# Kernel tuning notes

Measured on AMD Instinct MI355X. Metric: run time of the kernel, lower is better.

The kernel has to match this reference:

```python
import jax, jax.numpy as jnp
import numpy as np

B, N, DIN, DOUT = 1, 8192, 256, 256
EPS = 1e-8

def setup_inputs() -> dict:
    key = jax.random.key(0)
    kA, kX, k1, k2, k3, k4 = jax.random.split(key, 6)
    A = jax.random.uniform(kA, (B, N, N), dtype=jnp.float32)          # dense adjacency [B,N,N]
    X = jax.random.normal(kX, (B, N, DIN), dtype=jnp.float32)          # node features [B,N,Din]
    s1 = 1.0 / np.sqrt(DIN)
    s2 = 1.0 / np.sqrt(DIN + DOUT)
    W_w = jax.random.uniform(k1, (DIN, DOUT), jnp.float32, -s1, s1)
    b_w = jax.random.uniform(k2, (DOUT,), jnp.float32, -s1, s1)
    W_fc = jax.random.uniform(k3, (DIN + DOUT, DOUT), jnp.float32, -s2, s2)
    b_fc = jax.random.uniform(k4, (DOUT,), jnp.float32, -s2, s2)
    return {"A": A, "X": X, "W_w": W_w, "b_w": b_w, "W_fc": W_fc, "b_fc": b_fc}

def reference(A, X, W_w, b_w, W_fc, b_fc):
    # inputs = relu(weight(X))  [B,N,Dout]
    h = jax.nn.relu(jnp.einsum('bnd,de->bne', X, W_w) + b_w)
    # A[...,None] * inputs[:,None] summed over neighbor dim == matmul (avg pooling)
    pooled = jnp.einsum('bij,bjd->bid', A, h)                # [B,N,Dout]
    size = jnp.sum(A, axis=2, keepdims=True) + EPS           # [B,N,1]
    pooled = pooled / size
    cat = jnp.concatenate([X, pooled], axis=-1)              # [B,N,Din+Dout]
    out = jax.nn.relu(jnp.einsum('bnd,de->bne', cat, W_fc) + b_fc) + EPS
    out = out / (jnp.linalg.norm(out) + EPS)                 # global L2 norm over all elements
    return out
```

## Files before the change

kernel.cpp:

```cpp
#include <hip/hip_runtime.h>
#include <hip/hip_bf16.h>
#include <math.h>

typedef __bf16 bf16;
typedef bf16 bf16x8 __attribute__((ext_vector_type(8)));
typedef bf16 bf16x4 __attribute__((ext_vector_type(4)));
typedef float f32x4 __attribute__((ext_vector_type(4)));

#define N_NODES 8192
#define DIN 256
#define DOUT 256
#define KCAT 512
#define EPSF 1e-8f
#define KSPLIT 4
#define KBLK 2048
#define BM 64
#define BK 32
#define NT (KBLK / BK)
#define BBASE 4096
#define BUFSZ 20480

__device__ __forceinline__ f32x4 mfma16(bf16x8 a, bf16x8 b, f32x4 c) {
    return __builtin_amdgcn_mfma_f32_16x16x32_bf16(a, b, c, 0, 0, 0);
}

#define WAITVM(N) asm volatile("s_waitcnt vmcnt(" #N ")" ::: "memory")
#define WAITLGKM  asm volatile("s_waitcnt lgkmcnt(0)" ::: "memory")
#define BAR       __builtin_amdgcn_s_barrier()

__global__ __launch_bounds__(256) void k0_prep(const float* __restrict__ Ww,
                                               const float* __restrict__ Wfc,
                                               bf16* __restrict__ WwT,
                                               bf16* __restrict__ WfcT) {
    int tid = blockIdx.x * 256 + threadIdx.x;
    if (tid < 256 * 256) {
        int n = tid >> 8, k = tid & 255;
        WwT[n * 256 + k] = (bf16)Ww[k * 256 + n];
    }
    if (tid < 256 * 512) {
        int n = tid >> 9, k = tid & 511;
        WfcT[n * 512 + k] = (bf16)Wfc[k * 256 + n];
    }
}

__global__ __launch_bounds__(128) void k1_h(const float* __restrict__ X,
                                            const bf16* __restrict__ WwT,
                                            const float* __restrict__ bw,
                                            bf16* __restrict__ hT) {
    const int lane = threadIdx.x & 63;
    const int wid  = threadIdx.x >> 6;
    const int m0   = blockIdx.x * 16;
    const int lrow = lane & 15;
    const int lk8  = (lane >> 4) * 8;

    f32x4 acc[8];
#pragma unroll
    for (int i = 0; i < 8; ++i) acc[i] = {0.f, 0.f, 0.f, 0.f};

#pragma unroll
    for (int ks = 0; ks < DIN; ks += 32) {
        const float* xp = X + (size_t)(m0 + lrow) * DIN + ks + lk8;
        f32x4 x0 = *reinterpret_cast<const f32x4*>(xp);
        f32x4 x1 = *reinterpret_cast<const f32x4*>(xp + 4);
        bf16x8 a;
#pragma unroll
        for (int j = 0; j < 4; ++j) { a[j] = (bf16)x0[j]; a[4 + j] = (bf16)x1[j]; }
#pragma unroll
        for (int nb = 0; nb < 8; ++nb) {
            int col = wid * 128 + nb * 16 + lrow;
            bf16x8 b = *reinterpret_cast<const bf16x8*>(WwT + (size_t)col * DIN + ks + lk8);
            acc[nb] = mfma16(a, b, acc[nb]);
        }
    }
    const int mrow = m0 + (lane >> 4) * 4;
#pragma unroll
    for (int nb = 0; nb < 8; ++nb) {
        int col = wid * 128 + nb * 16 + lrow;
        float bias = bw[col];
        bf16x4 hv;
#pragma unroll
        for (int j = 0; j < 4; ++j) {
            float v = acc[nb][j] + bias;
            hv[j] = (bf16)(v > 0.f ? v : 0.f);
        }
        *reinterpret_cast<bf16x4*>(hT + (size_t)col * N_NODES + mrow) = hv;
    }
}

__global__ __launch_bounds__(512, 4) void k2_pool(const float* __restrict__ A,
                                                  const bf16* __restrict__ hT,
                                                  float* __restrict__ part,
                                                  float* __restrict__ rsG) {
    __shared__ __align__(16) unsigned char lds[2][BUFSZ];
    __shared__ float rsp[4][BM];
    const int t    = threadIdx.x;
    const int lane = t & 63;
    const int wid  = t >> 6;
    const int wr   = wid >> 2;
    const int wn   = wid & 3;
    const int lrow = lane & 15;
    const int lk4  = lane >> 4;
    const int mblk = blockIdx.x & 127;
    const int ks   = blockIdx.x >> 7;
    const int m0   = mblk * BM;
    const int kbase = ks * KBLK;

    f32x4 acc[2][4];
    f32x4 sums[2];
#pragma unroll
    for (int i = 0; i < 2; ++i) {
        sums[i] = {0.f, 0.f, 0.f, 0.f};
#pragma unroll
        for (int j = 0; j < 4; ++j) acc[i][j] = {0.f, 0.f, 0.f, 0.f};
    }
    bf16x8 bOne;
#pragma unroll
    for (int j = 0; j < 8; ++j) bOne[j] = (bf16)1.0f;

    const int arow = t >> 3;
    const int apos = t & 7;
    const float* aSrc = A + (size_t)(m0 + arow) * N_NODES + kbase + apos * 4;
    const int awb = arow * 64 + ((((apos >> 1) ^ ((arow >> 1) & 3))) << 4) + (apos & 1) * 8;

    const bf16* bsrc[2];
    int bdst[2];
#pragma unroll
    for (int r = 0; r < 2; ++r) {
        int idx = r * 512 + t;
        int col = idx >> 2;
        int gs  = (idx & 3) ^ ((col >> 1) & 3);
        bsrc[r] = hT + (size_t)col * N_NODES + kbase + gs * 8;
        bdst[r] = BBASE + r * 8192 + wid * 1024;
    }

    int aOff[2], bOff[4];
#pragma unroll
    for (int mf = 0; mf < 2; ++mf) {
        int row = wr * 32 + mf * 16 + lrow;
        aOff[mf] = row * 64 + ((lk4 ^ ((row >> 1) & 3)) << 4);
    }
#pragma unroll
    for (int nf = 0; nf < 4; ++nf) {
        int col = wn * 64 + nf * 16 + lrow;
        bOff[nf] = BBASE + col * 64 + ((lk4 ^ ((col >> 1) & 3)) << 4);
    }

    f32x4 ra;

#define ALOAD(tile) do { ra = *reinterpret_cast<const f32x4*>(aSrc + (size_t)(tile) * BK); } while (0)

#define CVTWRITE(bufidx) do {                                                 \
        bf16x4 w_;                                                            \
        _Pragma("unroll")                                                     \
        for (int j = 0; j < 4; ++j) w_[j] = (bf16)ra[j];                      \
        *reinterpret_cast<bf16x4*>(&lds[bufidx][awb]) = w_;                   \
    } while (0)

#define BDMA(tile, bufidx) do {                                               \
        _Pragma("unroll")                                                     \
        for (int r_ = 0; r_ < 2; ++r_) {                                      \
            __builtin_amdgcn_global_load_lds(                                 \
                (const __attribute__((address_space(1))) void*)(bsrc[r_] + (size_t)(tile) * BK), \
                (__attribute__((address_space(3))) void*)&lds[bufidx][bdst[r_]], \
                16, 0, 0);                                                    \
        }                                                                     \
    } while (0)

#define COMPUTE(bufidx, tile) do {                                            \
        bf16x8 af_[2], bf_[4];                                                \
        _Pragma("unroll")                                                     \
        for (int f = 0; f < 2; ++f)                                           \
            af_[f] = *reinterpret_cast<const bf16x8*>(&lds[bufidx][aOff[f]]); \
        _Pragma("unroll")                                                     \
        for (int f = 0; f < 4; ++f)                                           \
            bf_[f] = *reinterpret_cast<const bf16x8*>(&lds[bufidx][bOff[f]]); \
        _Pragma("unroll")                                                     \
        for (int mf = 0; mf < 2; ++mf)                                        \
            _Pragma("unroll")                                                 \
            for (int nf = 0; nf < 4; ++nf)                                    \
                acc[mf][nf] = mfma16(af_[mf], bf_[nf], acc[mf][nf]);          \
        if (wn == ((tile) & 3)) {                                             \
            sums[0] = mfma16(af_[0], bOne, sums[0]);                          \
            sums[1] = mfma16(af_[1], bOne, sums[1]);                          \
        }                                                                     \
    } while (0)

    ALOAD(0); BDMA(0, 0);
    CVTWRITE(0);
    ALOAD(1); BDMA(1, 1);
    WAITVM(3);
    WAITLGKM;
    BAR;

    for (int tt = 0; tt < NT - 2; ++tt) {
        CVTWRITE((tt + 1) & 1);
        COMPUTE(tt & 1, tt);
        ALOAD(tt + 2);
        WAITVM(1);
        WAITLGKM;
        BAR;
        BDMA(tt + 2, tt & 1);
    }
    CVTWRITE((NT - 1) & 1);
    COMPUTE((NT - 2) & 1, NT - 2);
    WAITVM(0);
    WAITLGKM;
    BAR;
    COMPUTE((NT - 1) & 1, NT - 1);

    if (lrow == 0) {
#pragma unroll
        for (int mf = 0; mf < 2; ++mf)
#pragma unroll
            for (int j = 0; j < 4; ++j)
                rsp[wn][wr * 32 + mf * 16 + lk4 * 4 + j] = sums[mf][j];
    }
    __syncthreads();
    if (t < BM)
        rsG[(size_t)ks * N_NODES + m0 + t] = rsp[0][t] + rsp[1][t] + rsp[2][t] + rsp[3][t];

    float* pp = part + ((size_t)ks * N_NODES + m0) * DOUT;
#pragma unroll
    for (int mf = 0; mf < 2; ++mf)
#pragma unroll
        for (int nf = 0; nf < 4; ++nf) {
            int col = wn * 64 + nf * 16 + lrow;
#pragma unroll
            for (int j = 0; j < 4; ++j) {
                int row = wr * 32 + mf * 16 + lk4 * 4 + j;
                pp[(size_t)row * DOUT + col] = acc[mf][nf][j];
            }
        }
#undef ALOAD
#undef CVTWRITE
#undef BDMA
#undef COMPUTE
}

__global__ __launch_bounds__(256) void k2b_combine(const float* __restrict__ part,
                                                   const float* __restrict__ rsG,
                                                   bf16* __restrict__ pooled) {
    int fl  = blockIdx.x * 256 + threadIdx.x;
    int row = fl >> 6;
    int c4  = (fl & 63) * 4;
    f32x4 s = {0.f, 0.f, 0.f, 0.f};
#pragma unroll
    for (int ks = 0; ks < KSPLIT; ++ks) {
        f32x4 v = *reinterpret_cast<const f32x4*>(part + ((size_t)ks * N_NODES + row) * DOUT + c4);
#pragma unroll
        for (int j = 0; j < 4; ++j) s[j] += v[j];
    }
    float rs = EPSF;
#pragma unroll
    for (int ks = 0; ks < KSPLIT; ++ks) rs += rsG[(size_t)ks * N_NODES + row];
    float inv = 1.f / rs;
    bf16x4 o;
#pragma unroll
    for (int j = 0; j < 4; ++j) o[j] = (bf16)(s[j] * inv);
    *reinterpret_cast<bf16x4*>(pooled + (size_t)row * DOUT + c4) = o;
}

__global__ __launch_bounds__(128) void k3_out(const float* __restrict__ X,
                                              const bf16* __restrict__ pooled,
                                              const bf16* __restrict__ WfcT,
                                              const float* __restrict__ bfc,
                                              float* __restrict__ out,
                                              float* __restrict__ partials) {
    const int lane = threadIdx.x & 63;
    const int wid  = threadIdx.x >> 6;
    const int m0   = blockIdx.x * 16;
    const int lrow = lane & 15;
    const int lk8  = (lane >> 4) * 8;

    f32x4 acc[8];
#pragma unroll
    for (int i = 0; i < 8; ++i) acc[i] = {0.f, 0.f, 0.f, 0.f};

#pragma unroll
    for (int ks = 0; ks < 256; ks += 32) {
        const float* xp = X + (size_t)(m0 + lrow) * DIN + ks + lk8;
        f32x4 x0 = *reinterpret_cast<const f32x4*>(xp);
        f32x4 x1 = *reinterpret_cast<const f32x4*>(xp + 4);
        bf16x8 a;
#pragma unroll
        for (int j = 0; j < 4; ++j) { a[j] = (bf16)x0[j]; a[4 + j] = (bf16)x1[j]; }
#pragma unroll
        for (int nb = 0; nb < 8; ++nb) {
            int col = wid * 128 + nb * 16 + lrow;
            bf16x8 b = *reinterpret_cast<const bf16x8*>(WfcT + (size_t)col * KCAT + ks + lk8);
            acc[nb] = mfma16(a, b, acc[nb]);
        }
    }
#pragma unroll
    for (int ks = 256; ks < 512; ks += 32) {
        bf16x8 a = *reinterpret_cast<const bf16x8*>(pooled + (size_t)(m0 + lrow) * DOUT + (ks - 256) + lk8);
#pragma unroll
        for (int nb = 0; nb < 8; ++nb) {
            int col = wid * 128 + nb * 16 + lrow;
            bf16x8 b = *reinterpret_cast<const bf16x8*>(WfcT + (size_t)col * KCAT + ks + lk8);
            acc[nb] = mfma16(a, b, acc[nb]);
        }
    }

    float ss = 0.f;
#pragma unroll
    for (int nb = 0; nb < 8; ++nb) {
        int col = wid * 128 + nb * 16 + lrow;
        float bias = bfc[col];
#pragma unroll
        for (int j = 0; j < 4; ++j) {
            int row = m0 + (lane >> 4) * 4 + j;
            float v = acc[nb][j] + bias;
            v = (v > 0.f ? v : 0.f) + EPSF;
            out[(size_t)row * DOUT + col] = v;
            ss += v * v;
        }
    }
#pragma unroll
    for (int off = 32; off; off >>= 1) ss += __shfl_xor(ss, off);
    __shared__ float sw[2];
    if (lane == 0) sw[wid] = ss;
    __syncthreads();
    if (threadIdx.x == 0) partials[blockIdx.x] = sw[0] + sw[1];
}

__global__ __launch_bounds__(256) void k4_norm(float* __restrict__ out,
                                               const float* __restrict__ partials) {
    __shared__ float sw[4];
    float s = partials[threadIdx.x] + partials[threadIdx.x + 256];
#pragma unroll
    for (int off = 32; off; off >>= 1) s += __shfl_xor(s, off);
    if ((threadIdx.x & 63) == 0) sw[threadIdx.x >> 6] = s;
    __syncthreads();
    float total = sw[0] + sw[1] + sw[2] + sw[3];
    float scale = 1.f / (sqrtf(total) + EPSF);
    f32x4* o4 = reinterpret_cast<f32x4*>(out);
    const int nvec = N_NODES * DOUT / 4;
    for (int i = blockIdx.x * blockDim.x + threadIdx.x; i < nvec; i += gridDim.x * blockDim.x) {
        f32x4 v = o4[i];
#pragma unroll
        for (int j = 0; j < 4; ++j) v[j] *= scale;
        o4[i] = v;
    }
}

extern "C" void kernel_launch(void* const* d_in, const int* in_sizes, int n_in,
                              void* d_out, int out_size, void* d_ws, size_t ws_size,
                              hipStream_t stream) {
    const float* A   = (const float*)d_in[0];
    const float* X   = (const float*)d_in[1];
    const float* Ww  = (const float*)d_in[2];
    const float* bw  = (const float*)d_in[3];
    const float* Wfc = (const float*)d_in[4];
    const float* bfc = (const float*)d_in[5];
    float* out = (float*)d_out;

    char* ws = (char*)d_ws;
    bf16*  hT        = (bf16*)(ws);
    bf16*  pooled    = (bf16*)(ws + (4u << 20));
    bf16*  WwT       = (bf16*)(ws + (8u << 20));
    bf16*  WfcT      = (bf16*)(ws + (8u << 20) + (128u << 10));
    float* partials  = (float*)(ws + (8u << 20) + (384u << 10));
    float* rsG       = (float*)(ws + (8u << 20) + (512u << 10));
    float* part      = (float*)(ws + (16u << 20));

    k0_prep<<<512, 256, 0, stream>>>(Ww, Wfc, WwT, WfcT);
    k1_h<<<512, 128, 0, stream>>>(X, WwT, bw, hT);
    k2_pool<<<512, 512, 0, stream>>>(A, hT, part, rsG);
    k2b_combine<<<N_NODES * DOUT / 1024, 256, 0, stream>>>(part, rsG, pooled);
    k3_out<<<512, 128, 0, stream>>>(X, pooled, WfcT, bfc, out, partials);
    k4_norm<<<256, 256, 0, stream>>>(out, partials);
}
```

Before: 162.3 us.

## Enlarge pool tile to 128 rows, deepen pipeline, fuse split-K combine into output GEMM

Doubles the k2_pool M tile to 128 rows so each hT tile staged in LDS is reused across twice as many rows. The LDS pipeline grows to 4 stages, with A register prefetch three tiles deep and wider 8-element A loads. The separate combine kernel is removed: k3_out now sums the four split-K partials, applies the row-sum normalization and converts to bf16 on the fly, which drops one launch and the pooled round trip. In exchange k2_pool uses more registers and LDS, has lower occupancy (launch bounds 2) and only 256 blocks, and k3_out reads fp32 partials redundantly across its two waves.

```diff
diff --git a/kernel.cpp b/kernel.cpp
--- a/kernel.cpp
+++ b/kernel.cpp
@@ -14,11 +14,11 @@
 #define EPSF 1e-8f
 #define KSPLIT 4
 #define KBLK 2048
-#define BM 64
+#define BM 128
 #define BK 32
 #define NT (KBLK / BK)
-#define BBASE 4096
-#define BUFSZ 20480
+#define STAGE 24576
+#define BBASE 8192
 
 __device__ __forceinline__ f32x4 mfma16(bf16x8 a, bf16x8 b, f32x4 c) {
     return __builtin_amdgcn_mfma_f32_16x16x32_bf16(a, b, c, 0, 0, 0);
@@ -87,11 +87,11 @@
     }
 }
 
-__global__ __launch_bounds__(512, 4) void k2_pool(const float* __restrict__ A,
+__global__ __launch_bounds__(512, 2) void k2_pool(const float* __restrict__ A,
                                                   const bf16* __restrict__ hT,
                                                   float* __restrict__ part,
                                                   float* __restrict__ rsG) {
-    __shared__ __align__(16) unsigned char lds[2][BUFSZ];
+    __shared__ __align__(16) unsigned char lds[4][STAGE];
     __shared__ float rsp[4][BM];
     const int t    = threadIdx.x;
     const int lane = t & 63;
@@ -100,15 +100,15 @@
     const int wn   = wid & 3;
     const int lrow = lane & 15;
     const int lk4  = lane >> 4;
-    const int mblk = blockIdx.x & 127;
-    const int ks   = blockIdx.x >> 7;
+    const int mblk = blockIdx.x & 63;
+    const int ks   = blockIdx.x >> 6;
     const int m0   = mblk * BM;
     const int kbase = ks * KBLK;
 
-    f32x4 acc[2][4];
-    f32x4 sums[2];
-#pragma unroll
-    for (int i = 0; i < 2; ++i) {
+    f32x4 acc[4][4];
+    f32x4 sums[4];
+#pragma unroll
+    for (int i = 0; i < 4; ++i) {
         sums[i] = {0.f, 0.f, 0.f, 0.f};
 #pragma unroll
         for (int j = 0; j < 4; ++j) acc[i][j] = {0.f, 0.f, 0.f, 0.f};
@@ -117,10 +117,10 @@
 #pragma unroll
     for (int j = 0; j < 8; ++j) bOne[j] = (bf16)1.0f;
 
-    const int arow = t >> 3;
-    const int apos = t & 7;
-    const float* aSrc = A + (size_t)(m0 + arow) * N_NODES + kbase + apos * 4;
-    const int awb = arow * 64 + ((((apos >> 1) ^ ((arow >> 1) & 3))) << 4) + (apos & 1) * 8;
+    const int arow = t >> 2;
+    const int aseg = t & 3;
+    const float* aSrc = A + (size_t)(m0 + arow) * N_NODES + kbase + aseg * 8;
+    const int awb = arow * 64 + ((aseg ^ ((arow >> 1) & 3)) << 4);
 
     const bf16* bsrc[2];
     int bdst[2];
@@ -133,10 +133,10 @@
         bdst[r] = BBASE + r * 8192 + wid * 1024;
     }
 
-    int aOff[2], bOff[4];
-#pragma unroll
-    for (int mf = 0; mf < 2; ++mf) {
-        int row = wr * 32 + mf * 16 + lrow;
+    int aOff[4], bOff[4];
+#pragma unroll
+    for (int mf = 0; mf < 4; ++mf) {
+        int row = wr * 64 + mf * 16 + lrow;
         aOff[mf] = row * 64 + ((lk4 ^ ((row >> 1) & 3)) << 4);
     }
 #pragma unroll
@@ -145,15 +145,21 @@
         bOff[nf] = BBASE + col * 64 + ((lk4 ^ ((col >> 1) & 3)) << 4);
     }
 
-    f32x4 ra;
-
-#define ALOAD(tile) do { ra = *reinterpret_cast<const f32x4*>(aSrc + (size_t)(tile) * BK); } while (0)
-
-#define CVTWRITE(bufidx) do {                                                 \
-        bf16x4 w_;                                                            \
-        _Pragma("unroll")                                                     \
-        for (int j = 0; j < 4; ++j) w_[j] = (bf16)ra[j];                      \
-        *reinterpret_cast<bf16x4*>(&lds[bufidx][awb]) = w_;                   \
+    f32x4 rlo[3], rhi[3];
+
+#define ALOAD(set, tile) do {                                                 \
+        const float* p_ = aSrc + (size_t)(tile) * BK;                         \
+        rlo[set] = *reinterpret_cast<const f32x4*>(p_);                       \
+        rhi[set] = *reinterpret_cast<const f32x4*>(p_ + 4);                   \
+    } while (0)
+
+#define CVTWRITE(set, bufidx) do {                                            \
+        bf16x8 w_;                                                            \
+        _Pragma("unroll")                                                     \
+        for (int j = 0; j < 4; ++j) {                                         \
+            w_[j] = (bf16)rlo[set][j]; w_[4 + j] = (bf16)rhi[set][j];         \
+        }                                                                     \
+        *reinterpret_cast<bf16x8*>(&lds[bufidx][awb]) = w_;                   \
     } while (0)
 
 #define BDMA(tile, bufidx) do {                                               \
@@ -167,53 +173,62 @@
     } while (0)
 
 #define COMPUTE(bufidx, tile) do {                                            \
-        bf16x8 af_[2], bf_[4];                                                \
-        _Pragma("unroll")                                                     \
-        for (int f = 0; f < 2; ++f)                                           \
+        bf16x8 af_[4], bf_[4];                                                \
+        _Pragma("unroll")                                                     \
+        for (int f = 0; f < 4; ++f)                                           \
             af_[f] = *reinterpret_cast<const bf16x8*>(&lds[bufidx][aOff[f]]); \
         _Pragma("unroll")                                                     \
         for (int f = 0; f < 4; ++f)                                           \
             bf_[f] = *reinterpret_cast<const bf16x8*>(&lds[bufidx][bOff[f]]); \
         _Pragma("unroll")                                                     \
-        for (int mf = 0; mf < 2; ++mf)                                        \
+        for (int mf = 0; mf < 4; ++mf)                                        \
             _Pragma("unroll")                                                 \
             for (int nf = 0; nf < 4; ++nf)                                    \
                 acc[mf][nf] = mfma16(af_[mf], bf_[nf], acc[mf][nf]);          \
         if (wn == ((tile) & 3)) {                                             \
-            sums[0] = mfma16(af_[0], bOne, sums[0]);                          \
-            sums[1] = mfma16(af_[1], bOne, sums[1]);                          \
+            _Pragma("unroll")                                                 \
+            for (int mf = 0; mf < 4; ++mf)                                    \
+                sums[mf] = mfma16(af_[mf], bOne, sums[mf]);                   \
         }                                                                     \
     } while (0)
 
-    ALOAD(0); BDMA(0, 0);
-    CVTWRITE(0);
-    ALOAD(1); BDMA(1, 1);
-    WAITVM(3);
+    ALOAD(0, 0); BDMA(0, 0);
+    ALOAD(1, 1); BDMA(1, 1);
+    ALOAD(2, 2); BDMA(2, 2);
+    CVTWRITE(0, 0);
+    ALOAD(0, 3);
+    WAITVM(10);
     WAITLGKM;
     BAR;
 
-    for (int tt = 0; tt < NT - 2; ++tt) {
-        CVTWRITE((tt + 1) & 1);
-        COMPUTE(tt & 1, tt);
-        ALOAD(tt + 2);
-        WAITVM(1);
+    for (int tt = 0; tt < NT - 3; ++tt) {
+        CVTWRITE((tt + 1) % 3, (tt + 1) & 3);
+        COMPUTE(tt & 3, tt);
+        BDMA(tt + 3, (tt + 3) & 3);
+        ALOAD((tt + 1) % 3, (tt + 4 < NT) ? (tt + 4) : 0);
+        WAITVM(10);
         WAITLGKM;
         BAR;
-        BDMA(tt + 2, tt & 1);
-    }
-    CVTWRITE((NT - 1) & 1);
-    COMPUTE((NT - 2) & 1, NT - 2);
-    WAITVM(0);
+    }
+    CVTWRITE((NT - 2) % 3, (NT - 2) & 3);
+    COMPUTE((NT - 3) & 3, NT - 3);
+    WAITVM(6);
     WAITLGKM;
     BAR;
-    COMPUTE((NT - 1) & 1, NT - 1);
-
+    CVTWRITE((NT - 1) % 3, (NT - 1) & 3);
+    COMPUTE((NT - 2) & 3, NT - 2);
+    WAITVM(2);
+    WAITLGKM;
+    BAR;
+    COMPUTE((NT - 1) & 3, NT - 1);
+
+    __syncthreads();
     if (lrow == 0) {
 #pragma unroll
-        for (int mf = 0; mf < 2; ++mf)
+        for (int mf = 0; mf < 4; ++mf)
 #pragma unroll
             for (int j = 0; j < 4; ++j)
-                rsp[wn][wr * 32 + mf * 16 + lk4 * 4 + j] = sums[mf][j];
+                rsp[wn][wr * 64 + mf * 16 + lk4 * 4 + j] = sums[mf][j];
     }
     __syncthreads();
     if (t < BM)
@@ -221,13 +236,13 @@
 
     float* pp = part + ((size_t)ks * N_NODES + m0) * DOUT;
 #pragma unroll
-    for (int mf = 0; mf < 2; ++mf)
+    for (int mf = 0; mf < 4; ++mf)
 #pragma unroll
         for (int nf = 0; nf < 4; ++nf) {
             int col = wn * 64 + nf * 16 + lrow;
 #pragma unroll
             for (int j = 0; j < 4; ++j) {
-                int row = wr * 32 + mf * 16 + lk4 * 4 + j;
+                int row = wr * 64 + mf * 16 + lk4 * 4 + j;
                 pp[(size_t)row * DOUT + col] = acc[mf][nf][j];
             }
         }
@@ -237,31 +252,9 @@
 #undef COMPUTE
 }
 
-__global__ __launch_bounds__(256) void k2b_combine(const float* __restrict__ part,
-                                                   const float* __restrict__ rsG,
-                                                   bf16* __restrict__ pooled) {
-    int fl  = blockIdx.x * 256 + threadIdx.x;
-    int row = fl >> 6;
-    int c4  = (fl & 63) * 4;
-    f32x4 s = {0.f, 0.f, 0.f, 0.f};
-#pragma unroll
-    for (int ks = 0; ks < KSPLIT; ++ks) {
-        f32x4 v = *reinterpret_cast<const f32x4*>(part + ((size_t)ks * N_NODES + row) * DOUT + c4);
-#pragma unroll
-        for (int j = 0; j < 4; ++j) s[j] += v[j];
-    }
-    float rs = EPSF;
-#pragma unroll
-    for (int ks = 0; ks < KSPLIT; ++ks) rs += rsG[(size_t)ks * N_NODES + row];
-    float inv = 1.f / rs;
-    bf16x4 o;
-#pragma unroll
-    for (int j = 0; j < 4; ++j) o[j] = (bf16)(s[j] * inv);
-    *reinterpret_cast<bf16x4*>(pooled + (size_t)row * DOUT + c4) = o;
-}
-
 __global__ __launch_bounds__(128) void k3_out(const float* __restrict__ X,
-                                              const bf16* __restrict__ pooled,
+                                              const float* __restrict__ part,
+                                              const float* __restrict__ rsG,
                                               const bf16* __restrict__ WfcT,
                                               const float* __restrict__ bfc,
                                               float* __restrict__ out,
@@ -276,9 +269,14 @@
 #pragma unroll
     for (int i = 0; i < 8; ++i) acc[i] = {0.f, 0.f, 0.f, 0.f};
 
-#pragma unroll
-    for (int ks = 0; ks < 256; ks += 32) {
-        const float* xp = X + (size_t)(m0 + lrow) * DIN + ks + lk8;
+    float rs = EPSF;
+#pragma unroll
+    for (int sp = 0; sp < KSPLIT; ++sp) rs += rsG[(size_t)sp * N_NODES + m0 + lrow];
+    const float inv = 1.f / rs;
+
+#pragma unroll
+    for (int ksx = 0; ksx < 256; ksx += 32) {
+        const float* xp = X + (size_t)(m0 + lrow) * DIN + ksx + lk8;
         f32x4 x0 = *reinterpret_cast<const f32x4*>(xp);
         f32x4 x1 = *reinterpret_cast<const f32x4*>(xp + 4);
         bf16x8 a;
@@ -287,17 +285,28 @@
 #pragma unroll
         for (int nb = 0; nb < 8; ++nb) {
             int col = wid * 128 + nb * 16 + lrow;
-            bf16x8 b = *reinterpret_cast<const bf16x8*>(WfcT + (size_t)col * KCAT + ks + lk8);
+            bf16x8 b = *reinterpret_cast<const bf16x8*>(WfcT + (size_t)col * KCAT + ksx + lk8);
             acc[nb] = mfma16(a, b, acc[nb]);
         }
     }
 #pragma unroll
-    for (int ks = 256; ks < 512; ks += 32) {
-        bf16x8 a = *reinterpret_cast<const bf16x8*>(pooled + (size_t)(m0 + lrow) * DOUT + (ks - 256) + lk8);
+    for (int ksx = 256; ksx < 512; ksx += 32) {
+        f32x4 s0 = {0.f, 0.f, 0.f, 0.f}, s1 = {0.f, 0.f, 0.f, 0.f};
+#pragma unroll
+        for (int sp = 0; sp < KSPLIT; ++sp) {
+            const float* pp = part + ((size_t)sp * N_NODES + m0 + lrow) * DOUT + (ksx - 256) + lk8;
+            f32x4 v0 = *reinterpret_cast<const f32x4*>(pp);
+            f32x4 v1 = *reinterpret_cast<const f32x4*>(pp + 4);
+#pragma unroll
+            for (int j = 0; j < 4; ++j) { s0[j] += v0[j]; s1[j] += v1[j]; }
+        }
+        bf16x8 a;
+#pragma unroll
+        for (int j = 0; j < 4; ++j) { a[j] = (bf16)(s0[j] * inv); a[4 + j] = (bf16)(s1[j] * inv); }
 #pragma unroll
         for (int nb = 0; nb < 8; ++nb) {
             int col = wid * 128 + nb * 16 + lrow;
-            bf16x8 b = *reinterpret_cast<const bf16x8*>(WfcT + (size_t)col * KCAT + ks + lk8);
+            bf16x8 b = *reinterpret_cast<const bf16x8*>(WfcT + (size_t)col * KCAT + ksx + lk8);
             acc[nb] = mfma16(a, b, acc[nb]);
         }
     }
@@ -357,7 +366,6 @@
 
     char* ws = (char*)d_ws;
     bf16*  hT        = (bf16*)(ws);
-    bf16*  pooled    = (bf16*)(ws + (4u << 20));
     bf16*  WwT       = (bf16*)(ws + (8u << 20));
     bf16*  WfcT      = (bf16*)(ws + (8u << 20) + (128u << 10));
     float* partials  = (float*)(ws + (8u << 20) + (384u << 10));
@@ -366,8 +374,7 @@
 
     k0_prep<<<512, 256, 0, stream>>>(Ww, Wfc, WwT, WfcT);
     k1_h<<<512, 128, 0, stream>>>(X, WwT, bw, hT);
-    k2_pool<<<512, 512, 0, stream>>>(A, hT, part, rsG);
-    k2b_combine<<<N_NODES * DOUT / 1024, 256, 0, stream>>>(part, rsG, pooled);
-    k3_out<<<512, 128, 0, stream>>>(X, pooled, WfcT, bfc, out, partials);
+    k2_pool<<<256, 512, 0, stream>>>(A, hT, part, rsG);
+    k3_out<<<512, 128, 0, stream>>>(X, part, rsG, WfcT, bfc, out, partials);
     k4_norm<<<256, 256, 0, stream>>>(out, partials);
 }
```

Result: slower. 168.9 us (+4.1%).
